# Kernel optimization log

Measured on AMD Instinct MI355X. Metric: run time of the kernel, lower is better.

Reference implementation:

```python
import jax, jax.numpy as jnp
import numpy as np

# model_grid_shape (flipped ensemble grid, all equal here); E = 8 experts
GRID = (2, 2, 2)
E = GRID[0] * GRID[1] * GRID[2]
N = 524288   # query points
H = 64       # sub-model MLP hidden width


def setup_inputs() -> dict:
    key = jax.random.key(0)
    ks = jax.random.split(key, 4)
    # query coordinates in [-1, 1]^3
    x = jax.random.uniform(ks[0], (N, 3), jnp.float32, -1.0, 1.0)
    # per-expert spatial extents: axis-aligned cells tiling [-1,1]^3, in the
    # same flat order as the routing index i0 + i1*g0 + i2*g0*g1
    i = np.arange(E)
    cell = np.stack([i % GRID[0], (i // GRID[0]) % GRID[1],
                     i // (GRID[0] * GRID[1])], axis=-1).astype(np.float32)
    g = np.array(GRID, np.float32)
    extents_min = jnp.asarray(-1.0 + 2.0 * cell / g)          # [E, 3]
    extents_max = jnp.asarray(-1.0 + 2.0 * (cell + 1.0) / g)  # [E, 3]
    # per-expert SRN MLP parameters: 3 -> H -> H -> 1
    W1 = jax.random.normal(ks[1], (E, 3, H), jnp.float32) / np.sqrt(3.0)
    b1 = jnp.zeros((E, H), jnp.float32)
    W2 = jax.random.normal(ks[2], (E, H, H), jnp.float32) / np.sqrt(float(H))
    b2 = jnp.zeros((E, H), jnp.float32)
    W3 = jax.random.normal(ks[3], (E, H, 1), jnp.float32) / np.sqrt(float(H))
    b3 = jnp.zeros((E, 1), jnp.float32)
    return {"x": x, "extents_min": extents_min, "extents_max": extents_max,
            "W1": W1, "b1": b1, "W2": W2, "b2": b2, "W3": W3, "b3": b3}


def reference(x, extents_min, extents_max, W1, b1, W2, b2, W3, b3):
    # --- routing: flat expert index per point (matches torch forward) ---
    u = jnp.clip((x + 1.0) * 0.5, 0.0, 0.99)
    gvec = jnp.asarray(GRID, x.dtype)
    gi = (u * gvec).astype(jnp.int32)                       # [N, 3]
    idx = gi[:, 0] + gi[:, 1] * GRID[0] + gi[:, 2] * (GRID[0] * GRID[1])

    # --- dispatch/combine: scan over experts, masked scatter into y ---
    def body(y, args):
        i, emin, emax, w1, bb1, w2, bb2, w3, bb3 = args
        # normalize point into expert-local [-1, 1]^3
        xn = -1.0 + 2.0 * ((x - emin) / (emax - emin))      # [N, 3]
        h = jax.nn.relu(xn @ w1 + bb1)                      # [N, H]
        h = jax.nn.relu(h @ w2 + bb2)                       # [N, H]
        o = h @ w3 + bb3                                    # [N, 1]
        mask = (idx == i)[:, None]
        return jnp.where(mask, o, y), None

    y0 = jnp.zeros((x.shape[0], 1), x.dtype)
    y, _ = jax.lax.scan(
        body, y0,
        (jnp.arange(E), extents_min, extents_max, W1, b1, W2, b2, W3, b3))
    return y
```

## Files before the change

### kernel.cpp

```cpp
#include <hip/hip_runtime.h>

typedef __bf16 bf16x8 __attribute__((ext_vector_type(8)));
typedef __bf16 bf16x2 __attribute__((ext_vector_type(2)));
typedef float f32x4 __attribute__((ext_vector_type(4)));
typedef float f32x2 __attribute__((ext_vector_type(2)));

#define N_PTS 524288
#define SBLK 256
#define PTS_PER_SBLK 2048
#define CAP 73728
#define POISON 0xAAAAAAAAu

__device__ __forceinline__ unsigned short f2bf(float f) {
    unsigned u = __float_as_uint(f);
    u += 0x7FFFu + ((u >> 16) & 1u);
    return (unsigned short)(u >> 16);
}

__device__ __forceinline__ unsigned decode(unsigned c) {
    return (c >= POISON) ? (c - POISON) : c;
}

__device__ __forceinline__ int route(float x0, float x1, float x2) {
    int g0 = (int)(fminf(fmaxf((x0 + 1.0f) * 0.5f, 0.0f), 0.99f) * 2.0f);
    int g1 = (int)(fminf(fmaxf((x1 + 1.0f) * 0.5f, 0.0f), 0.99f) * 2.0f);
    int g2 = (int)(fminf(fmaxf((x2 + 1.0f) * 0.5f, 0.0f), 0.99f) * 2.0f);
    return g0 + 2*g1 + 4*g2;
}

#define OFF_CNT  0u
#define OFF_XG   1024u

extern "C" __global__ void __launch_bounds__(256) k3_scatter(
        const float* __restrict__ x, int* __restrict__ cursor,
        float4* __restrict__ xg) {
    __shared__ int lh[8];
    __shared__ int startS[8];
    int t = threadIdx.x;
    if (t < 8) lh[t] = 0;
    __syncthreads();
    int base = blockIdx.x * PTS_PER_SBLK;
    float c0[8], c1[8], c2[8];
    unsigned epack = 0;
    #pragma unroll
    for (int i = 0; i < 8; ++i) {
        int p = base + i * 256 + t;
        c0[i] = x[3*p]; c1[i] = x[3*p+1]; c2[i] = x[3*p+2];
        int e = route(c0[i], c1[i], c2[i]);
        epack |= (unsigned)e << (3*i);
        atomicAdd(&lh[e], 1);
    }
    __syncthreads();
    if (t < 8) {
        unsigned claim = (unsigned)atomicAdd(&cursor[t], lh[t]);
        startS[t] = (int)decode(claim);
        lh[t] = 0;
    }
    __syncthreads();
    #pragma unroll
    for (int i = 0; i < 8; ++i) {
        int e = (epack >> (3*i)) & 7;
        int r = atomicAdd(&lh[e], 1);
        float4 v;
        v.x = c0[i]; v.y = c1[i]; v.z = c2[i];
        v.w = __uint_as_float((unsigned)(base + i * 256 + t));
        xg[e*CAP + startS[e] + r] = v;
    }
}

extern "C" __global__ void __launch_bounds__(256, 3) k4_mlp(
        const float4* __restrict__ xg, const int* __restrict__ cursor,
        const float* __restrict__ emin, const float* __restrict__ emax,
        const float* __restrict__ W1, const float* __restrict__ b1,
        const float* __restrict__ W2, const float* __restrict__ b2,
        const float* __restrict__ W3, const float* __restrict__ b3,
        float* __restrict__ y) {
    int e = blockIdx.y;
    int cnt = (int)decode((unsigned)cursor[e]);
    int tileStart = blockIdx.x * 256;
    if (tileStart >= cnt) return;
    int base = e * CAP;

    int t = threadIdx.x;
    int lane = t & 63, wave = t >> 6;
    int m16 = lane & 15;
    int g  = lane >> 4;
    int g8 = g * 8;

    __shared__ __align__(16) unsigned short h1s[256][72];
    __shared__ __align__(16) unsigned short w2t[64][72];
    __shared__ float4 w1s[64];
    __shared__ float  b2s[64], w3s[64];

    if (t < 64) {
        int n = t;
        float d0 = emax[e*3+0] - emin[e*3+0];
        float d1 = emax[e*3+1] - emin[e*3+1];
        float d2 = emax[e*3+2] - emin[e*3+2];
        float a0 = 2.0f/d0, a1 = 2.0f/d1, a2 = 2.0f/d2;
        float cc0 = -1.0f - 2.0f*emin[e*3+0]/d0;
        float cc1 = -1.0f - 2.0f*emin[e*3+1]/d1;
        float cc2 = -1.0f - 2.0f*emin[e*3+2]/d2;
        float w0 = W1[(e*3+0)*64 + n];
        float w1 = W1[(e*3+1)*64 + n];
        float w2 = W1[(e*3+2)*64 + n];
        float4 w;
        w.x = a0*w0; w.y = a1*w1; w.z = a2*w2;
        w.w = cc0*w0 + cc1*w1 + cc2*w2 + b1[e*64 + n];
        w1s[n] = w;
    } else if (t < 128) {
        b2s[t - 64]  = b2[e*64 + (t - 64)];
    } else if (t < 192) {
        w3s[t - 128] = W3[e*64 + (t - 128)];
    }
    #pragma unroll
    for (int i = 0; i < 16; ++i) {
        int idx = i * 256 + t;
        int k = idx >> 6, n = idx & 63;
        w2t[n][k] = f2bf(W2[(e*64 + k)*64 + n]);
    }

    int valid = (tileStart + t) < cnt;
    float px = 0.f, py = 0.f, pz = 0.f;
    unsigned pidx = 0;
    if (valid) {
        float4 v = xg[base + tileStart + t];
        px = v.x; py = v.y; pz = v.z; pidx = __float_as_uint(v.w);
    }
    __syncthreads();

    #pragma unroll
    for (int jb = 0; jb < 8; ++jb) {
        bf16x8 hv;
        #pragma unroll
        for (int j2 = 0; j2 < 8; j2 += 2) {
            float4 wa = w1s[jb*8 + j2];
            float4 wb = w1s[jb*8 + j2 + 1];
            float ha = fmaf(px, wa.x, fmaf(py, wa.y, fmaf(pz, wa.z, wa.w)));
            float hb = fmaf(px, wb.x, fmaf(py, wb.y, fmaf(pz, wb.z, wb.w)));
            f32x2 hp;
            hp[0] = fmaxf(ha, 0.0f);
            hp[1] = fmaxf(hb, 0.0f);
            bf16x2 bp = __builtin_convertvector(hp, bf16x2);
            hv[j2] = bp[0]; hv[j2+1] = bp[1];
        }
        *(bf16x8*)(&h1s[t][jb*8]) = hv;
    }
    __syncthreads();

    bf16x8 A[4][2];
    #pragma unroll
    for (int mt = 0; mt < 4; ++mt)
        #pragma unroll
        for (int kt = 0; kt < 2; ++kt)
            A[mt][kt] = *(const bf16x8*)(&w2t[mt*16 + m16][kt*32 + g8]);

    f32x4 acc[4][4] = {};
    #pragma unroll
    for (int pt = 0; pt < 4; ++pt) {
        int row = wave*64 + pt*16 + m16;
        bf16x8 B0 = *(const bf16x8*)(&h1s[row][g8]);
        bf16x8 B1 = *(const bf16x8*)(&h1s[row][32 + g8]);
        #pragma unroll
        for (int mt = 0; mt < 4; ++mt) {
            acc[mt][pt] = __builtin_amdgcn_mfma_f32_16x16x32_bf16(A[mt][0], B0, acc[mt][pt], 0, 0, 0);
            acc[mt][pt] = __builtin_amdgcn_mfma_f32_16x16x32_bf16(A[mt][1], B1, acc[mt][pt], 0, 0, 0);
        }
    }

    float bb3 = b3[e];
    #pragma unroll
    for (int pt = 0; pt < 4; ++pt) {
        float s = 0.0f;
        #pragma unroll
        for (int mt = 0; mt < 4; ++mt) {
            #pragma unroll
            for (int r = 0; r < 4; ++r) {
                int f = mt*16 + g*4 + r;
                float h2 = fmaxf(acc[mt][pt][r] + b2s[f], 0.0f);
                s = fmaf(h2, w3s[f], s);
            }
        }
        s += __shfl_xor(s, 16, 64);
        s += __shfl_xor(s, 32, 64);
        unsigned oi = (unsigned)__shfl((int)pidx, pt*16 + m16, 64);
        int row = wave*64 + pt*16 + m16;
        if (lane < 16 && (tileStart + row) < cnt) {
            y[oi] = s + bb3;
        }
    }
}

extern "C" void kernel_launch(void* const* d_in, const int* in_sizes, int n_in,
                              void* d_out, int out_size, void* d_ws, size_t ws_size,
                              hipStream_t stream) {
    const float* x    = (const float*)d_in[0];
    const float* emin = (const float*)d_in[1];
    const float* emax = (const float*)d_in[2];
    const float* W1   = (const float*)d_in[3];
    const float* b1   = (const float*)d_in[4];
    const float* W2   = (const float*)d_in[5];
    const float* b2   = (const float*)d_in[6];
    const float* W3   = (const float*)d_in[7];
    const float* b3   = (const float*)d_in[8];
    float* y = (float*)d_out;

    char* ws = (char*)d_ws;
    int*  cursor = (int*)(ws + OFF_CNT);
    float4* xg   = (float4*)(ws + OFF_XG);

    k3_scatter<<<SBLK, 256, 0, stream>>>(x, cursor, xg);
    k4_mlp<<<dim3(288, 8), 256, 0, stream>>>(xg, cursor, emin, emax,
                                             W1, b1, W2, b2, W3, b3, y);
}
```

Baseline: 95.79 us.

## Precompute per-expert weight fragments in scatter kernel and drop MLP-kernel LDS staging

Adds 8 extra blocks to the scatter kernel that precompute each expert's folded W1/bias, packed b2/W3 pairs, and W2 already converted to bf16 in MFMA fragment order, then writes them to workspace. The MLP kernel loads A fragments directly from global memory and reads W1P/EP through the cache, which removes the per-block W2 transpose/convert, the weight shared-memory staging and one __syncthreads. The scatter kernel also keeps the rank from its first shared atomic so the second round of atomics is no longer needed. In exchange, the MLP kernel now issues more global/scalar loads per block. It also relies on a manual lgkmcnt wait in place of a barrier before reading h1s, which is only safe because each wave reads rows written by its own threads.

```diff
diff --git a/kernel.cpp b/kernel.cpp
--- a/kernel.cpp
+++ b/kernel.cpp
@@ -29,18 +29,65 @@
 }
 
 #define OFF_CNT  0u
-#define OFF_XG   1024u
+#define OFF_W1P  1024u
+#define OFF_EP   10240u
+#define OFF_W2F  16384u
+#define OFF_XG   131072u
 
 extern "C" __global__ void __launch_bounds__(256) k3_scatter(
         const float* __restrict__ x, int* __restrict__ cursor,
-        float4* __restrict__ xg) {
+        float4* __restrict__ xg,
+        const float* __restrict__ emin, const float* __restrict__ emax,
+        const float* __restrict__ W1, const float* __restrict__ b1,
+        const float* __restrict__ W2, const float* __restrict__ b2,
+        const float* __restrict__ W3,
+        float4* __restrict__ W1P, float2* __restrict__ EP,
+        uint4* __restrict__ W2F) {
+    int t = threadIdx.x;
+
+    if (blockIdx.x >= SBLK) {
+        int e = blockIdx.x - SBLK;
+        if (t < 64) {
+            int n = t;
+            float d0 = emax[e*3+0] - emin[e*3+0];
+            float d1 = emax[e*3+1] - emin[e*3+1];
+            float d2 = emax[e*3+2] - emin[e*3+2];
+            float a0 = 2.0f/d0, a1 = 2.0f/d1, a2 = 2.0f/d2;
+            float cc0 = -1.0f - 2.0f*emin[e*3+0]/d0;
+            float cc1 = -1.0f - 2.0f*emin[e*3+1]/d1;
+            float cc2 = -1.0f - 2.0f*emin[e*3+2]/d2;
+            float w0 = W1[(e*3+0)*64 + n];
+            float w1 = W1[(e*3+1)*64 + n];
+            float w2 = W1[(e*3+2)*64 + n];
+            float4 w;
+            w.x = a0*w0; w.y = a1*w1; w.z = a2*w2;
+            w.w = cc0*w0 + cc1*w1 + cc2*w2 + b1[e*64 + n];
+            W1P[e*64 + n] = w;
+            EP[e*64 + n] = make_float2(b2[e*64 + n], W3[e*64 + n]);
+        }
+        #pragma unroll
+        for (int s = 0; s < 2; ++s) {
+            int q  = s*256 + t;
+            int fi = q >> 6, l = q & 63;
+            int mt = fi >> 1, kt = fi & 1;
+            int n  = mt*16 + (l & 15);
+            int g8 = (l >> 4) * 8;
+            union { unsigned short us[8]; uint4 u4; } v;
+            #pragma unroll
+            for (int j = 0; j < 8; ++j)
+                v.us[j] = f2bf(W2[(e*64 + kt*32 + g8 + j)*64 + n]);
+            W2F[(e*8 + fi)*64 + l] = v.u4;
+        }
+        return;
+    }
+
     __shared__ int lh[8];
     __shared__ int startS[8];
-    int t = threadIdx.x;
     if (t < 8) lh[t] = 0;
     __syncthreads();
     int base = blockIdx.x * PTS_PER_SBLK;
     float c0[8], c1[8], c2[8];
+    int rnk[8];
     unsigned epack = 0;
     #pragma unroll
     for (int i = 0; i < 8; ++i) {
@@ -48,38 +95,33 @@
         c0[i] = x[3*p]; c1[i] = x[3*p+1]; c2[i] = x[3*p+2];
         int e = route(c0[i], c1[i], c2[i]);
         epack |= (unsigned)e << (3*i);
-        atomicAdd(&lh[e], 1);
+        rnk[i] = atomicAdd(&lh[e], 1);
     }
     __syncthreads();
     if (t < 8) {
         unsigned claim = (unsigned)atomicAdd(&cursor[t], lh[t]);
         startS[t] = (int)decode(claim);
-        lh[t] = 0;
     }
     __syncthreads();
     #pragma unroll
     for (int i = 0; i < 8; ++i) {
         int e = (epack >> (3*i)) & 7;
-        int r = atomicAdd(&lh[e], 1);
         float4 v;
         v.x = c0[i]; v.y = c1[i]; v.z = c2[i];
         v.w = __uint_as_float((unsigned)(base + i * 256 + t));
-        xg[e*CAP + startS[e] + r] = v;
+        xg[e*CAP + startS[e] + rnk[i]] = v;
     }
 }
 
 extern "C" __global__ void __launch_bounds__(256, 3) k4_mlp(
         const float4* __restrict__ xg, const int* __restrict__ cursor,
-        const float* __restrict__ emin, const float* __restrict__ emax,
-        const float* __restrict__ W1, const float* __restrict__ b1,
-        const float* __restrict__ W2, const float* __restrict__ b2,
-        const float* __restrict__ W3, const float* __restrict__ b3,
+        const float4* __restrict__ W1P, const float2* __restrict__ EP,
+        const bf16x8* __restrict__ W2F, const float* __restrict__ b3,
         float* __restrict__ y) {
     int e = blockIdx.y;
     int cnt = (int)decode((unsigned)cursor[e]);
     int tileStart = blockIdx.x * 256;
     if (tileStart >= cnt) return;
-    int base = e * CAP;
 
     int t = threadIdx.x;
     int lane = t & 63, wave = t >> 6;
@@ -88,54 +130,29 @@
     int g8 = g * 8;
 
     __shared__ __align__(16) unsigned short h1s[256][72];
-    __shared__ __align__(16) unsigned short w2t[64][72];
-    __shared__ float4 w1s[64];
-    __shared__ float  b2s[64], w3s[64];
-
-    if (t < 64) {
-        int n = t;
-        float d0 = emax[e*3+0] - emin[e*3+0];
-        float d1 = emax[e*3+1] - emin[e*3+1];
-        float d2 = emax[e*3+2] - emin[e*3+2];
-        float a0 = 2.0f/d0, a1 = 2.0f/d1, a2 = 2.0f/d2;
-        float cc0 = -1.0f - 2.0f*emin[e*3+0]/d0;
-        float cc1 = -1.0f - 2.0f*emin[e*3+1]/d1;
-        float cc2 = -1.0f - 2.0f*emin[e*3+2]/d2;
-        float w0 = W1[(e*3+0)*64 + n];
-        float w1 = W1[(e*3+1)*64 + n];
-        float w2 = W1[(e*3+2)*64 + n];
-        float4 w;
-        w.x = a0*w0; w.y = a1*w1; w.z = a2*w2;
-        w.w = cc0*w0 + cc1*w1 + cc2*w2 + b1[e*64 + n];
-        w1s[n] = w;
-    } else if (t < 128) {
-        b2s[t - 64]  = b2[e*64 + (t - 64)];
-    } else if (t < 192) {
-        w3s[t - 128] = W3[e*64 + (t - 128)];
-    }
-    #pragma unroll
-    for (int i = 0; i < 16; ++i) {
-        int idx = i * 256 + t;
-        int k = idx >> 6, n = idx & 63;
-        w2t[n][k] = f2bf(W2[(e*64 + k)*64 + n]);
-    }
+
+    bf16x8 A[4][2];
+    #pragma unroll
+    for (int mt = 0; mt < 4; ++mt)
+        #pragma unroll
+        for (int kt = 0; kt < 2; ++kt)
+            A[mt][kt] = W2F[(e*8 + mt*2 + kt)*64 + lane];
 
     int valid = (tileStart + t) < cnt;
     float px = 0.f, py = 0.f, pz = 0.f;
     unsigned pidx = 0;
     if (valid) {
-        float4 v = xg[base + tileStart + t];
+        float4 v = xg[e*CAP + tileStart + t];
         px = v.x; py = v.y; pz = v.z; pidx = __float_as_uint(v.w);
     }
-    __syncthreads();
 
     #pragma unroll
     for (int jb = 0; jb < 8; ++jb) {
         bf16x8 hv;
         #pragma unroll
         for (int j2 = 0; j2 < 8; j2 += 2) {
-            float4 wa = w1s[jb*8 + j2];
-            float4 wb = w1s[jb*8 + j2 + 1];
+            float4 wa = W1P[e*64 + jb*8 + j2];
+            float4 wb = W1P[e*64 + jb*8 + j2 + 1];
             float ha = fmaf(px, wa.x, fmaf(py, wa.y, fmaf(pz, wa.z, wa.w)));
             float hb = fmaf(px, wb.x, fmaf(py, wb.y, fmaf(pz, wb.z, wb.w)));
             f32x2 hp;
@@ -146,14 +163,8 @@
         }
         *(bf16x8*)(&h1s[t][jb*8]) = hv;
     }
-    __syncthreads();
-
-    bf16x8 A[4][2];
-    #pragma unroll
-    for (int mt = 0; mt < 4; ++mt)
-        #pragma unroll
-        for (int kt = 0; kt < 2; ++kt)
-            A[mt][kt] = *(const bf16x8*)(&w2t[mt*16 + m16][kt*32 + g8]);
+
+    asm volatile("s_waitcnt lgkmcnt(0)" ::: "memory");
 
     f32x4 acc[4][4] = {};
     #pragma unroll
@@ -168,19 +179,23 @@
         }
     }
 
+    float s0 = 0.f, s1 = 0.f, s2 = 0.f, s3 = 0.f;
+    #pragma unroll
+    for (int mt = 0; mt < 4; ++mt) {
+        #pragma unroll
+        for (int r = 0; r < 4; ++r) {
+            float2 ep = EP[e*64 + mt*16 + g*4 + r];
+            s0 = fmaf(fmaxf(acc[mt][0][r] + ep.x, 0.f), ep.y, s0);
+            s1 = fmaf(fmaxf(acc[mt][1][r] + ep.x, 0.f), ep.y, s1);
+            s2 = fmaf(fmaxf(acc[mt][2][r] + ep.x, 0.f), ep.y, s2);
+            s3 = fmaf(fmaxf(acc[mt][3][r] + ep.x, 0.f), ep.y, s3);
+        }
+    }
     float bb3 = b3[e];
+    float sv[4] = {s0, s1, s2, s3};
     #pragma unroll
     for (int pt = 0; pt < 4; ++pt) {
-        float s = 0.0f;
-        #pragma unroll
-        for (int mt = 0; mt < 4; ++mt) {
-            #pragma unroll
-            for (int r = 0; r < 4; ++r) {
-                int f = mt*16 + g*4 + r;
-                float h2 = fmaxf(acc[mt][pt][r] + b2s[f], 0.0f);
-                s = fmaf(h2, w3s[f], s);
-            }
-        }
+        float s = sv[pt];
         s += __shfl_xor(s, 16, 64);
         s += __shfl_xor(s, 32, 64);
         unsigned oi = (unsigned)__shfl((int)pidx, pt*16 + m16, 64);
@@ -206,10 +221,14 @@
     float* y = (float*)d_out;
 
     char* ws = (char*)d_ws;
-    int*  cursor = (int*)(ws + OFF_CNT);
-    float4* xg   = (float4*)(ws + OFF_XG);
-
-    k3_scatter<<<SBLK, 256, 0, stream>>>(x, cursor, xg);
-    k4_mlp<<<dim3(288, 8), 256, 0, stream>>>(xg, cursor, emin, emax,
-                                             W1, b1, W2, b2, W3, b3, y);
-}
+    int*    cursor = (int*)(ws + OFF_CNT);
+    float4* W1P    = (float4*)(ws + OFF_W1P);
+    float2* EP     = (float2*)(ws + OFF_EP);
+    uint4*  W2F    = (uint4*)(ws + OFF_W2F);
+    float4* xg     = (float4*)(ws + OFF_XG);
+
+    k3_scatter<<<SBLK + 8, 256, 0, stream>>>(x, cursor, xg, emin, emax,
+                                             W1, b1, W2, b2, W3, W1P, EP, W2F);
+    k4_mlp<<<dim3(288, 8), 256, 0, stream>>>(xg, cursor, W1P, EP,
+                                             (const bf16x8*)W2F, b3, y);
+}
```

New measurement: 94.66 us. About the same (-1.2%).
